# Optimization experiments

Measured on AMD Instinct MI355X. Metric: run time of the kernel, lower is better.

The kernel has to match this reference:

```python
import jax, jax.numpy as jnp
import numpy as np

NUM_HEAD = 8
NEG = -1e9

def _lin(x, W, b):
    return x @ W + b

def _attn(qx, kx, vx, mask, H):
    # qx:[B,S,D], kx/vx:[B,T,D], mask:[B,T] float (0/1). masked_fill BEFORE scale, per original.
    B, S, D = qx.shape
    T = kx.shape[1]
    dh = D // H
    qh = qx.reshape(B, S, H, dh).transpose(0, 2, 1, 3)
    kh = kx.reshape(B, T, H, dh).transpose(0, 2, 1, 3)
    vh = vx.reshape(B, T, H, dh).transpose(0, 2, 1, 3)
    s = jnp.einsum('bhsd,bhtd->bhst', qh, kh)
    s = jnp.where(mask[:, None, None, :] == 0, NEG, s) / jnp.sqrt(jnp.float32(dh))
    p = jax.nn.softmax(s, axis=-1)
    o = jnp.einsum('bhst,bhtd->bhsd', p, vh)
    return o.transpose(0, 2, 1, 3).reshape(B, S, D)

def _forward(v, q, c, v_mask, q_mask, c_mask,
             Wv4q, bv4q, Wq4v, bq4v, Wv, bv, Wq, bq, Wc, bc,
             m_v_k, m_v_v, m_c_k, m_c_v, Wvo, bvo, Wqo, bqo, Wco, bco):
    B = v.shape[0]
    D = Wvo.shape[0]
    H = NUM_HEAD
    # masked means -> gates
    v_mean = (v * v_mask[:, :, None]).sum(1) / v_mask.sum(1)[:, None]
    q_mean = (q * q_mask[:, :, None]).sum(1) / q_mask.sum(1)[:, None]
    v4q_gate = jax.nn.sigmoid(_lin(jax.nn.relu(v_mean), Wv4q, bv4q))[:, None, :]
    q4v_gate = jax.nn.sigmoid(_lin(jax.nn.relu(q_mean), Wq4v, bq4v))[:, None, :]
    # QKV projections (drop=0), masked
    v_trans = _lin(jax.nn.relu(v), Wv, bv) * v_mask[:, :, None]
    q_trans = _lin(jax.nn.relu(q), Wq, bq) * q_mask[:, :, None]
    c_trans = _lin(jax.nn.relu(c), Wc, bc) * c_mask[:, :, None]
    v_k, v_q, v_v = jnp.split(v_trans, 3, axis=2)
    q_k, q_q, q_v = jnp.split(q_trans, 3, axis=2)
    c_k, c_q, c_v = jnp.split(c_trans, 3, axis=2)
    # memory tokens: K scaled by sqrt(D), V scaled by sqrt(mv)=1 (faithful to original)
    sd = np.sqrt(D).astype(np.float32)
    m_vk = sd * jnp.broadcast_to(m_v_k, (B, 1, D))
    m_vv = 1.0 * jnp.broadcast_to(m_v_v, (B, 1, D))
    v_k = jnp.concatenate([m_vk, v_k], axis=1)
    v_v = jnp.concatenate([m_vv, v_v], axis=1)
    v_mask_m = jnp.concatenate([jnp.ones((B, 1), v_mask.dtype), v_mask], axis=1)
    m_ck = sd * jnp.broadcast_to(m_c_k, (B, 1, D))
    m_cv = 1.0 * jnp.broadcast_to(m_c_v, (B, 1, D))
    c_k = jnp.concatenate([m_ck, c_k], axis=1)
    c_v = jnp.concatenate([m_cv, c_v], axis=1)
    c_mask_m = jnp.concatenate([jnp.ones((B, 1), c_mask.dtype), c_mask], axis=1)
    # cross-modal gating of Q/K
    new_vq = (1 + q4v_gate) * v_q
    new_vk = (1 + q4v_gate) * v_k
    new_qq = (1 + v4q_gate) * q_q
    new_qk = (1 + v4q_gate) * q_k
    # multi-head attention (vectorized over heads; equivalent to the per-head loop)
    v_update = _attn(new_vq, new_vk, v_v, v_mask_m, H)
    q_update = _attn(new_qq, new_qk, q_v, q_mask, H)
    c_update = _attn(c_q, c_k, c_v, c_mask_m, H)
    updated_v = _lin(v + v_update, Wvo, bvo)
    updated_q = _lin(q + q_update, Wqo, bqo)
    updated_c = _lin(c + c_update, Wco, bco)
    return (updated_v, updated_q, updated_c)

def setup_inputs() -> dict:
    key = jax.random.key(0)
    ks = jax.random.split(key, 20)
    B, NO, ML, MLC, D = 32, 512, 256, 512, 1024
    s = 0.02
    def N(k, shape, sc=1.0):
        return jax.random.normal(k, shape, dtype=jnp.float32) * sc
    def M(k, b, S):
        m = (jax.random.uniform(k, (b, S)) < 0.85).astype(jnp.float32)
        return m.at[:, 0].set(1.0)  # guarantee nonzero mask sums
    return dict(
        v=N(ks[0], (B, NO, D)), q=N(ks[1], (B, ML, D)), c=N(ks[2], (B, MLC, D)),
        v_mask=M(ks[3], B, NO), q_mask=M(ks[4], B, ML), c_mask=M(ks[5], B, MLC),
        Wv4q=N(ks[6], (D, D), s), bv4q=jnp.zeros((D,), jnp.float32),
        Wq4v=N(ks[7], (D, D), s), bq4v=jnp.zeros((D,), jnp.float32),
        Wv=N(ks[8], (D, 3 * D), s), bv=jnp.zeros((3 * D,), jnp.float32),
        Wq=N(ks[9], (D, 3 * D), s), bq=jnp.zeros((3 * D,), jnp.float32),
        Wc=N(ks[10], (D, 3 * D), s), bc=jnp.zeros((3 * D,), jnp.float32),
        m_v_k=N(ks[11], (1, 1, D), s), m_v_v=N(ks[12], (1, 1, D), s),
        m_c_k=N(ks[13], (1, 1, D), s), m_c_v=N(ks[14], (1, 1, D), s),
        Wvo=N(ks[15], (D, D), s), bvo=jnp.zeros((D,), jnp.float32),
        Wqo=N(ks[16], (D, D), s), bqo=jnp.zeros((D,), jnp.float32),
        Wco=N(ks[17], (D, D), s), bco=jnp.zeros((D,), jnp.float32),
    )

def reference(v, q, c, v_mask, q_mask, c_mask,
              Wv4q, bv4q, Wq4v, bq4v, Wv, bv, Wq, bq, Wc, bc,
              m_v_k, m_v_v, m_c_k, m_c_v, Wvo, bvo, Wqo, bqo, Wco, bco):
    return _forward(v, q, c, v_mask, q_mask, c_mask,
                    Wv4q, bv4q, Wq4v, bq4v, Wv, bv, Wq, bq, Wc, bc,
                    m_v_k, m_v_v, m_c_k, m_c_v, Wvo, bvo, Wqo, bqo, Wco, bco)
```

## Files before the change

kernel.cpp:

```cpp
#include <hip/hip_runtime.h>
#include <hip/hip_bf16.h>

typedef __bf16 bf16;
typedef __bf16 bf16x8 __attribute__((ext_vector_type(8)));
typedef float  f32x4  __attribute__((ext_vector_type(4)));

__device__ __forceinline__ void gl2lds16(const bf16* g, bf16* l) {
    __builtin_amdgcn_global_load_lds((const __attribute__((address_space(1))) void*)g,
                                     (__attribute__((address_space(3))) void*)l,
                                     16, 0, 0);
}

__global__ void relu_cast_kernel(const float* __restrict__ x, bf16* __restrict__ y, int n8) {
    int i = blockIdx.x * 256 + threadIdx.x;
    if (i >= n8) return;
    const float4* xp = (const float4*)x + (size_t)i * 2;
    float4 a = xp[0], b = xp[1];
    bf16x8 o;
    o[0] = (bf16)fmaxf(a.x, 0.f); o[1] = (bf16)fmaxf(a.y, 0.f);
    o[2] = (bf16)fmaxf(a.z, 0.f); o[3] = (bf16)fmaxf(a.w, 0.f);
    o[4] = (bf16)fmaxf(b.x, 0.f); o[5] = (bf16)fmaxf(b.y, 0.f);
    o[6] = (bf16)fmaxf(b.z, 0.f); o[7] = (bf16)fmaxf(b.w, 0.f);
    *(bf16x8*)(y + (size_t)i * 8) = o;
}

__global__ void mean_kernel(const float* __restrict__ x, const float* __restrict__ mask,
                            float* __restrict__ mean, int S) {
    int b = blockIdx.y;
    int n = blockIdx.x * 256 + threadIdx.x;
    const float* xb = x + (size_t)b * S * 1024;
    const float* mb = mask + (size_t)b * S;
    float acc = 0.f, msum = 0.f;
    for (int s = 0; s < S; ++s) {
        float mk = mb[s];
        msum += mk;
        acc += mk * xb[(size_t)s * 1024 + n];
    }
    mean[b * 1024 + n] = acc / msum;
}

__global__ void gate_kernel(const float* __restrict__ mean, const float* __restrict__ W,
                            const float* __restrict__ bias, float* __restrict__ gate) {
    int b = blockIdx.y;
    int n = blockIdx.x * 256 + threadIdx.x;
    const float* mb = mean + b * 1024;
    float acc = 0.f;
    for (int k = 0; k < 1024; ++k) {
        float a = mb[k];
        a = a > 0.f ? a : 0.f;
        acc += a * W[(size_t)k * 1024 + n];
    }
    acc += bias[n];
    gate[b * 1024 + n] = 1.0f / (1.0f + __expf(-acc));
}

__global__ void transpose_kernel(const float* __restrict__ W, bf16* __restrict__ Wt,
                                 int K, int N) {
    __shared__ bf16 tile[32][33];
    int k0 = blockIdx.x * 32, n0 = blockIdx.y * 32;
    int tx = threadIdx.x, ty = threadIdx.y;
#pragma unroll
    for (int i = 0; i < 4; ++i)
        tile[ty * 4 + i][tx] = (bf16)W[(size_t)(k0 + ty * 4 + i) * N + n0 + tx];
    __syncthreads();
#pragma unroll
    for (int i = 0; i < 4; ++i)
        Wt[(size_t)(n0 + ty * 4 + i) * K + k0 + tx] = tile[tx][ty * 4 + i];
}

template <typename OutT>
__global__ void gemm_bt(const bf16* __restrict__ A, const bf16* __restrict__ Bt,
                        const float* __restrict__ bias, OutT* __restrict__ C,
                        int M, int N,
                        const float* __restrict__ mask,
                        const float* __restrict__ gate,
                        int s_shift)
{
    const int K = 1024;
    __shared__ __align__(16) bf16 Al[128 * 32];
    __shared__ __align__(16) bf16 Bl[128 * 32];

    int tid  = threadIdx.x;
    int lane = tid & 63, w = tid >> 6;
    int wm = w >> 1, wn = w & 1;
    int quad = lane >> 4, l16 = lane & 15;
    int bm = blockIdx.y, bn = blockIdx.x;

    const bf16* Ab = A  + (size_t)bm * 128 * K;
    const bf16* Bb = Bt + (size_t)bn * 128 * K;

    f32x4 acc[4][4];
    f32x4 zero = {0.f, 0.f, 0.f, 0.f};
#pragma unroll
    for (int i = 0; i < 4; ++i)
#pragma unroll
        for (int j = 0; j < 4; ++j) acc[i][j] = zero;

    for (int k0 = 0; k0 < K; k0 += 32) {
        __syncthreads();
#pragma unroll
        for (int p = 0; p < 2; ++p) {
            int c   = p * 256 + tid;
            int row = c >> 2, c8 = (c & 3) * 8;
            bf16* ldsb_a = Al + (size_t)(p * 256 + w * 64) * 8;
            bf16* ldsb_b = Bl + (size_t)(p * 256 + w * 64) * 8;
            gl2lds16(Ab + (size_t)row * K + k0 + c8, ldsb_a);
            gl2lds16(Bb + (size_t)row * K + k0 + c8, ldsb_b);
        }
        __syncthreads();

        bf16x8 af[4], bfr[4];
#pragma unroll
        for (int mt = 0; mt < 4; ++mt)
            af[mt] = *(const bf16x8*)&Al[(wm * 64 + mt * 16 + l16) * 32 + quad * 8];
#pragma unroll
        for (int nt = 0; nt < 4; ++nt)
            bfr[nt] = *(const bf16x8*)&Bl[(wn * 64 + nt * 16 + l16) * 32 + quad * 8];
#pragma unroll
        for (int mt = 0; mt < 4; ++mt)
#pragma unroll
            for (int nt = 0; nt < 4; ++nt)
                acc[mt][nt] = __builtin_amdgcn_mfma_f32_16x16x32_bf16(
                    af[mt], bfr[nt], acc[mt][nt], 0, 0, 0);
    }

#pragma unroll
    for (int mt = 0; mt < 4; ++mt) {
#pragma unroll
        for (int nt = 0; nt < 4; ++nt) {
#pragma unroll
            for (int r = 0; r < 4; ++r) {
                int mrow = bm * 128 + wm * 64 + mt * 16 + quad * 4 + r;
                int ncol = bn * 128 + wn * 64 + nt * 16 + l16;
                float v = acc[mt][nt][r] + bias[ncol];
                if (mask) {
                    v *= mask[mrow];
                    if (gate && ncol < 2048) {
                        int b = mrow >> s_shift;
                        v *= 1.0f + gate[b * 1024 + (ncol & 1023)];
                    }
                }
                C[(size_t)mrow * N + ncol] = (OutT)v;
            }
        }
    }
}

__global__ __launch_bounds__(256)
void attn_kernel(const bf16* __restrict__ trans, const float* __restrict__ X,
                 bf16* __restrict__ upd, const float* __restrict__ mask,
                 const float* __restrict__ gate,
                 const float* __restrict__ mvk, const float* __restrict__ mvv,
                 int S, int T0, int has_mem)
{
    const int T = T0 + has_mem;
    const size_t rs = 3072;
    __shared__ __align__(16) bf16 Kl[64 * 128];
    __shared__ __align__(16) bf16 Vt[128 * 72];
    __shared__ __align__(16) bf16 Pl[4 * 16 * 72];

    int tid  = threadIdx.x;
    int lane = tid & 63, w = tid >> 6;
    int quad = lane >> 4, l16 = lane & 15;
    int st = blockIdx.x, h = blockIdx.y, b = blockIdx.z;
    int s0 = st * 64;
    const bf16* Tb = trans + (size_t)b * S * rs;

    bf16x8 qf[4];
    {
        const bf16* qp = Tb + (size_t)(s0 + w * 16 + l16) * rs + 1024 + h * 128 + quad * 8;
#pragma unroll
        for (int kk = 0; kk < 4; ++kk)
            qf[kk] = *(const bf16x8*)(qp + kk * 32);
    }

    float m_st[4], l_st[4];
    f32x4 o_acc[8];
    f32x4 zero = {0.f, 0.f, 0.f, 0.f};
#pragma unroll
    for (int r = 0; r < 4; ++r) { m_st[r] = -3.0e38f; l_st[r] = 0.f; }
#pragma unroll
    for (int n = 0; n < 8; ++n) o_acc[n] = zero;

    const float inv_sqrt = 0.08838834764831845f;
    int nT = (T + 63) >> 6;
    for (int kt = 0; kt < nT; ++kt) {
        int t0 = kt * 64;
        __syncthreads();

#pragma unroll
        for (int p = 0; p < 4; ++p) {
            int c = p * 256 + tid;
            int row = c >> 4;
            int c16 = ((c & 15) ^ (row & 7)) * 8;
            int t = t0 + row;
            int sr = has_mem ? (t - 1) : t;
            sr = sr < 0 ? 0 : sr;
            sr = sr > T0 - 1 ? T0 - 1 : sr;
            gl2lds16(Tb + (size_t)sr * rs + h * 128 + c16,
                     Kl + (size_t)(p * 256 + w * 64) * 8);
        }
#pragma unroll
        for (int i = 0; i < 4; ++i) {
            int chunk = i * 256 + tid;
            int tl = chunk >> 4;
            int d8 = (chunk & 15) * 8;
            int t = t0 + tl;
            bf16 vbuf[8];
            if (has_mem && t == 0) {
                const float* mp = mvv + h * 128 + d8;
#pragma unroll
                for (int j = 0; j < 8; ++j) vbuf[j] = (bf16)mp[j];
            } else {
                int sr = has_mem ? (t - 1) : t;
                sr = sr < 0 ? 0 : sr;
                sr = sr > T0 - 1 ? T0 - 1 : sr;
                bf16x8 vv = *(const bf16x8*)(Tb + (size_t)sr * rs + 2048 + h * 128 + d8);
#pragma unroll
                for (int j = 0; j < 8; ++j) vbuf[j] = vv[j];
            }
            int tswz = (((tl >> 3) ^ ((d8 >> 3) & 7)) << 3) + (tl & 7);
#pragma unroll
            for (int j = 0; j < 8; ++j)
                Vt[(d8 + j) * 72 + tswz] = vbuf[j];
        }
        __syncthreads();

        if (has_mem && kt == 0 && tid < 128) {
            float g = gate ? (1.0f + gate[b * 1024 + h * 128 + tid]) : 1.0f;
            Kl[tid] = (bf16)(32.0f * mvk[h * 128 + tid] * g);
        }
        __syncthreads();

        f32x4 accs[4];
#pragma unroll
        for (int tt = 0; tt < 4; ++tt) accs[tt] = zero;
#pragma unroll
        for (int kc = 0; kc < 128; kc += 32) {
            bf16x8 aq = qf[kc >> 5];
#pragma unroll
            for (int tt = 0; tt < 4; ++tt) {
                bf16x8 bk = *(const bf16x8*)&Kl[(tt * 16 + l16) * 128 +
                                                ((((kc >> 3) + quad) ^ (l16 & 7)) << 3)];
                accs[tt] = __builtin_amdgcn_mfma_f32_16x16x32_bf16(aq, bk, accs[tt], 0, 0, 0);
            }
        }

        float sv[4][4];
#pragma unroll
        for (int tt = 0; tt < 4; ++tt) {
            int t = t0 + tt * 16 + l16;
            float mk;
            if (t >= T)        mk = 0.f;
            else if (has_mem)  mk = (t == 0) ? 1.f : mask[b * T0 + t - 1];
            else               mk = mask[b * T0 + t];
#pragma unroll
            for (int r = 0; r < 4; ++r) {
                float x = accs[tt][r];
                x = (mk != 0.f) ? x : -1e9f;
                sv[tt][r] = x * inv_sqrt;
            }
        }

#pragma unroll
        for (int r = 0; r < 4; ++r) {
            float mx = fmaxf(fmaxf(sv[0][r], sv[1][r]), fmaxf(sv[2][r], sv[3][r]));
#pragma unroll
            for (int off = 1; off < 16; off <<= 1)
                mx = fmaxf(mx, __shfl_xor(mx, off, 64));
            float m_new = fmaxf(m_st[r], mx);
            float alpha = __expf(m_st[r] - m_new);
            float rsum = 0.f;
#pragma unroll
            for (int tt = 0; tt < 4; ++tt) {
                float p = __expf(sv[tt][r] - m_new);
                sv[tt][r] = p;
                rsum += p;
            }
#pragma unroll
            for (int off = 1; off < 16; off <<= 1)
                rsum += __shfl_xor(rsum, off, 64);
            l_st[r] = l_st[r] * alpha + rsum;
            m_st[r] = m_new;
#pragma unroll
            for (int n = 0; n < 8; ++n) o_acc[n][r] *= alpha;
        }

#pragma unroll
        for (int tt = 0; tt < 4; ++tt)
#pragma unroll
            for (int r = 0; r < 4; ++r)
                Pl[w * 1152 + (quad * 4 + r) * 72 + tt * 16 + l16] = (bf16)sv[tt][r];
        __asm__ volatile("s_waitcnt lgkmcnt(0)" ::: "memory");

#pragma unroll
        for (int kc = 0; kc < 64; kc += 32) {
            bf16x8 ap = *(const bf16x8*)&Pl[w * 1152 + l16 * 72 + kc + quad * 8];
#pragma unroll
            for (int n = 0; n < 8; ++n) {
                int d = n * 16 + l16;
                int ct = ((kc >> 3) + quad) ^ ((d >> 3) & 7);
                bf16x8 bv = *(const bf16x8*)&Vt[d * 72 + (ct << 3)];
                o_acc[n] = __builtin_amdgcn_mfma_f32_16x16x32_bf16(ap, bv, o_acc[n], 0, 0, 0);
            }
        }
    }

#pragma unroll
    for (int n = 0; n < 8; ++n) {
#pragma unroll
        for (int r = 0; r < 4; ++r) {
            int s = s0 + w * 16 + quad * 4 + r;
            int d = n * 16 + l16;
            size_t off = (size_t)(b * S + s) * 1024 + h * 128 + d;
            float val = o_acc[n][r] / l_st[r];
            upd[off] = (bf16)(X[off] + val);
        }
    }
}

extern "C" void kernel_launch(void* const* d_in, const int* in_sizes, int n_in,
                              void* d_out, int out_size, void* d_ws, size_t ws_size,
                              hipStream_t stream) {
    (void)in_sizes; (void)n_in; (void)out_size; (void)ws_size;
    const float* v      = (const float*)d_in[0];
    const float* q      = (const float*)d_in[1];
    const float* c      = (const float*)d_in[2];
    const float* v_mask = (const float*)d_in[3];
    const float* q_mask = (const float*)d_in[4];
    const float* c_mask = (const float*)d_in[5];
    const float* Wv4q = (const float*)d_in[6];
    const float* bv4q = (const float*)d_in[7];
    const float* Wq4v = (const float*)d_in[8];
    const float* bq4v = (const float*)d_in[9];
    const float* Wv   = (const float*)d_in[10];
    const float* bv   = (const float*)d_in[11];
    const float* Wq   = (const float*)d_in[12];
    const float* bq   = (const float*)d_in[13];
    const float* Wc   = (const float*)d_in[14];
    const float* bc   = (const float*)d_in[15];
    const float* mvk  = (const float*)d_in[16];
    const float* mvv  = (const float*)d_in[17];
    const float* mck  = (const float*)d_in[18];
    const float* mcv  = (const float*)d_in[19];
    const float* Wvo  = (const float*)d_in[20];
    const float* bvo  = (const float*)d_in[21];
    const float* Wqo  = (const float*)d_in[22];
    const float* bqo  = (const float*)d_in[23];
    const float* Wco  = (const float*)d_in[24];
    const float* bco  = (const float*)d_in[25];
    float* out = (float*)d_out;

    char* ws = (char*)d_ws;
    size_t o = 0;
    bf16*  reluV  = (bf16*)(ws + o); o += (size_t)16384 * 1024 * 2;
    bf16*  reluQ  = (bf16*)(ws + o); o += (size_t)8192  * 1024 * 2;
    bf16*  reluC  = (bf16*)(ws + o); o += (size_t)16384 * 1024 * 2;
    bf16*  WtV    = (bf16*)(ws + o); o += (size_t)3072 * 1024 * 2;
    bf16*  WtQ    = (bf16*)(ws + o); o += (size_t)3072 * 1024 * 2;
    bf16*  WtC    = (bf16*)(ws + o); o += (size_t)3072 * 1024 * 2;
    bf16*  WtVO   = (bf16*)(ws + o); o += (size_t)1024 * 1024 * 2;
    bf16*  WtQO   = (bf16*)(ws + o); o += (size_t)1024 * 1024 * 2;
    bf16*  WtCO   = (bf16*)(ws + o); o += (size_t)1024 * 1024 * 2;
    bf16*  transV = (bf16*)(ws + o); o += (size_t)16384 * 3072 * 2;
    bf16*  transQ = (bf16*)(ws + o); o += (size_t)8192  * 3072 * 2;
    bf16*  transC = (bf16*)(ws + o); o += (size_t)16384 * 3072 * 2;
    float* meanV  = (float*)(ws + o); o += (size_t)32 * 1024 * 4;
    float* meanQ  = (float*)(ws + o); o += (size_t)32 * 1024 * 4;
    float* gV4Q   = (float*)(ws + o); o += (size_t)32 * 1024 * 4;
    float* gQ4V   = (float*)(ws + o); o += (size_t)32 * 1024 * 4;
    bf16* updV = reluV;
    bf16* updQ = reluQ;
    bf16* updC = reluC;

    relu_cast_kernel<<<8192, 256, 0, stream>>>(v, reluV, 2097152);
    relu_cast_kernel<<<4096, 256, 0, stream>>>(q, reluQ, 1048576);
    relu_cast_kernel<<<8192, 256, 0, stream>>>(c, reluC, 2097152);

    mean_kernel<<<dim3(4, 32), 256, 0, stream>>>(v, v_mask, meanV, 512);
    mean_kernel<<<dim3(4, 32), 256, 0, stream>>>(q, q_mask, meanQ, 256);

    gate_kernel<<<dim3(4, 32), 256, 0, stream>>>(meanV, Wv4q, bv4q, gV4Q);
    gate_kernel<<<dim3(4, 32), 256, 0, stream>>>(meanQ, Wq4v, bq4v, gQ4V);

    transpose_kernel<<<dim3(32, 96), dim3(32, 8), 0, stream>>>(Wv,  WtV,  1024, 3072);
    transpose_kernel<<<dim3(32, 96), dim3(32, 8), 0, stream>>>(Wq,  WtQ,  1024, 3072);
    transpose_kernel<<<dim3(32, 96), dim3(32, 8), 0, stream>>>(Wc,  WtC,  1024, 3072);
    transpose_kernel<<<dim3(32, 32), dim3(32, 8), 0, stream>>>(Wvo, WtVO, 1024, 1024);
    transpose_kernel<<<dim3(32, 32), dim3(32, 8), 0, stream>>>(Wqo, WtQO, 1024, 1024);
    transpose_kernel<<<dim3(32, 32), dim3(32, 8), 0, stream>>>(Wco, WtCO, 1024, 1024);

    gemm_bt<bf16><<<dim3(24, 128), 256, 0, stream>>>(reluV, WtV, bv, transV, 16384, 3072, v_mask, gQ4V, 9);
    gemm_bt<bf16><<<dim3(24, 64),  256, 0, stream>>>(reluQ, WtQ, bq, transQ, 8192,  3072, q_mask, gV4Q, 8);
    gemm_bt<bf16><<<dim3(24, 128), 256, 0, stream>>>(reluC, WtC, bc, transC, 16384, 3072, c_mask, nullptr, 9);

    attn_kernel<<<dim3(8, 8, 32), 256, 0, stream>>>(transV, v, updV, v_mask, gQ4V, mvk, mvv, 512, 512, 1);
    attn_kernel<<<dim3(4, 8, 32), 256, 0, stream>>>(transQ, q, updQ, q_mask, nullptr, nullptr, nullptr, 256, 256, 0);
    attn_kernel<<<dim3(8, 8, 32), 256, 0, stream>>>(transC, c, updC, c_mask, nullptr, mck, mcv, 512, 512, 1);

    gemm_bt<float><<<dim3(8, 128), 256, 0, stream>>>(updV, WtVO, bvo, out,            16384, 1024, nullptr, nullptr, 0);
    gemm_bt<float><<<dim3(8, 64),  256, 0, stream>>>(updQ, WtQO, bqo, out + 16777216, 8192,  1024, nullptr, nullptr, 0);
    gemm_bt<float><<<dim3(8, 128), 256, 0, stream>>>(updC, WtCO, bco, out + 25165824, 16384, 1024, nullptr, nullptr, 0);
}
```

Baseline: 1.657 ms.

## Replace 128x128 GEMM with double-buffered 256x256 tile GEMM using swizzled LDS

The 128x128 single-buffered GEMM is replaced by a 256x256-tile kernel with 512 threads and 8x4 MFMA fragments per wave. It uses double-buffered LDS staging over a K step of 64, split into two 32-wide halves, with vmcnt-based barriers so the next tile's loads overlap the current MFMAs. It also adds an XOR swizzle on LDS columns and raises wave priority around the MFMA blocks. The goal is more data reuse per byte loaded, hidden global-load latency and fewer bank conflicts, at the cost of higher register pressure and fewer blocks for the small Q GEMMs.

```diff
diff --git a/kernel.cpp b/kernel.cpp
--- a/kernel.cpp
+++ b/kernel.cpp
@@ -9,6 +9,17 @@
     __builtin_amdgcn_global_load_lds((const __attribute__((address_space(1))) void*)g,
                                      (__attribute__((address_space(3))) void*)l,
                                      16, 0, 0);
+}
+
+__device__ __forceinline__ void vm_bar4() {
+    asm volatile("s_waitcnt vmcnt(4)" ::: "memory");
+    __builtin_amdgcn_s_barrier();
+    asm volatile("" ::: "memory");
+}
+__device__ __forceinline__ void vm_bar0() {
+    asm volatile("s_waitcnt vmcnt(0)" ::: "memory");
+    __builtin_amdgcn_s_barrier();
+    asm volatile("" ::: "memory");
 }
 
 __global__ void relu_cast_kernel(const float* __restrict__ x, bf16* __restrict__ y, int n8) {
@@ -69,78 +80,113 @@
 }
 
 template <typename OutT>
-__global__ void gemm_bt(const bf16* __restrict__ A, const bf16* __restrict__ Bt,
-                        const float* __restrict__ bias, OutT* __restrict__ C,
-                        int M, int N,
-                        const float* __restrict__ mask,
-                        const float* __restrict__ gate,
-                        int s_shift)
+__global__ __launch_bounds__(512, 2)
+void gemm256(const bf16* __restrict__ A, const bf16* __restrict__ Bt,
+             const float* __restrict__ bias, OutT* __restrict__ C,
+             int N,
+             const float* __restrict__ mask,
+             const float* __restrict__ gate,
+             int s_shift)
 {
-    const int K = 1024;
-    __shared__ __align__(16) bf16 Al[128 * 32];
-    __shared__ __align__(16) bf16 Bl[128 * 32];
-
-    int tid  = threadIdx.x;
-    int lane = tid & 63, w = tid >> 6;
-    int wm = w >> 1, wn = w & 1;
-    int quad = lane >> 4, l16 = lane & 15;
-    int bm = blockIdx.y, bn = blockIdx.x;
-
-    const bf16* Ab = A  + (size_t)bm * 128 * K;
-    const bf16* Bb = Bt + (size_t)bn * 128 * K;
-
-    f32x4 acc[4][4];
+    constexpr int KD = 1024;
+    constexpr int NT = 16;
+    __shared__ __align__(16) bf16 Ls[2][2][2][8192];
+
+    const int tid  = threadIdx.x;
+    const int lane = tid & 63, w = tid >> 6;
+    const int wm = w >> 2, wn = w & 3;
+    const int quad = lane >> 4, l16 = lane & 15;
+    const int bn = blockIdx.x, bm = blockIdx.y;
+
+    const bf16* Ab = A  + (size_t)bm * 256 * KD;
+    const bf16* Bb = Bt + (size_t)bn * 256 * KD;
+
+    const int srow   = tid >> 2;
+    const int schunk = tid & 3;
+    const int scol   = ((schunk ^ ((srow >> 1) & 3)) << 3);
+    const bf16* gA0 = Ab + (size_t)srow * KD + scol;
+    const bf16* gB0 = Bb + (size_t)srow * KD + scol;
+    const int ldst = w * 512;
+
+    const int cswz = ((quad ^ ((l16 >> 1) & 3)) << 3);
+    const int aoff = (wm * 128 + l16) * 32 + cswz;
+    const int boff = (wn * 64  + l16) * 32 + cswz;
+
+    f32x4 acc[8][4];
     f32x4 zero = {0.f, 0.f, 0.f, 0.f};
 #pragma unroll
-    for (int i = 0; i < 4; ++i)
+    for (int i = 0; i < 8; ++i)
 #pragma unroll
         for (int j = 0; j < 4; ++j) acc[i][j] = zero;
 
-    for (int k0 = 0; k0 < K; k0 += 32) {
-        __syncthreads();
-#pragma unroll
-        for (int p = 0; p < 2; ++p) {
-            int c   = p * 256 + tid;
-            int row = c >> 2, c8 = (c & 3) * 8;
-            bf16* ldsb_a = Al + (size_t)(p * 256 + w * 64) * 8;
-            bf16* ldsb_b = Bl + (size_t)(p * 256 + w * 64) * 8;
-            gl2lds16(Ab + (size_t)row * K + k0 + c8, ldsb_a);
-            gl2lds16(Bb + (size_t)row * K + k0 + c8, ldsb_b);
-        }
-        __syncthreads();
-
-        bf16x8 af[4], bfr[4];
-#pragma unroll
-        for (int mt = 0; mt < 4; ++mt)
-            af[mt] = *(const bf16x8*)&Al[(wm * 64 + mt * 16 + l16) * 32 + quad * 8];
-#pragma unroll
-        for (int nt = 0; nt < 4; ++nt)
-            bfr[nt] = *(const bf16x8*)&Bl[(wn * 64 + nt * 16 + l16) * 32 + quad * 8];
-#pragma unroll
-        for (int mt = 0; mt < 4; ++mt)
-#pragma unroll
-            for (int nt = 0; nt < 4; ++nt)
-                acc[mt][nt] = __builtin_amdgcn_mfma_f32_16x16x32_bf16(
-                    af[mt], bfr[nt], acc[mt][nt], 0, 0, 0);
-    }
-
-#pragma unroll
-    for (int mt = 0; mt < 4; ++mt) {
-#pragma unroll
-        for (int nt = 0; nt < 4; ++nt) {
+    auto STAGE = [&](int buf, int kk, int t) {
+        const bf16* ga = gA0 + t * 64 + kk * 32;
+        const bf16* gb = gB0 + t * 64 + kk * 32;
+        bf16* la = &Ls[buf][0][kk][ldst];
+        bf16* lb = &Ls[buf][1][kk][ldst];
+        gl2lds16(ga,              la);
+        gl2lds16(ga + 128 * KD,   la + 4096);
+        gl2lds16(gb,              lb);
+        gl2lds16(gb + 128 * KD,   lb + 4096);
+    };
+
+    auto COMPUTE = [&](int buf, int kk) {
+        const bf16* Ak = &Ls[buf][0][kk][0];
+        const bf16* Bk = &Ls[buf][1][kk][0];
+        bf16x8 af[8], bv[4];
+#pragma unroll
+        for (int mf = 0; mf < 8; ++mf)
+            af[mf] = *(const bf16x8*)&Ak[aoff + mf * 512];
+#pragma unroll
+        for (int nf = 0; nf < 4; ++nf)
+            bv[nf] = *(const bf16x8*)&Bk[boff + nf * 512];
+        __builtin_amdgcn_s_setprio(1);
+#pragma unroll
+        for (int mf = 0; mf < 8; ++mf)
+#pragma unroll
+            for (int nf = 0; nf < 4; ++nf)
+                acc[mf][nf] = __builtin_amdgcn_mfma_f32_16x16x32_bf16(
+                    af[mf], bv[nf], acc[mf][nf], 0, 0, 0);
+        __builtin_amdgcn_s_setprio(0);
+    };
+
+    STAGE(0, 0, 0);
+    STAGE(0, 1, 0);
+    vm_bar4();
+
+    int buf = 0;
+    for (int t = 0; t < NT - 1; ++t) {
+        STAGE(buf ^ 1, 0, t + 1);
+        COMPUTE(buf, 0);
+        vm_bar4();
+        STAGE(buf ^ 1, 1, t + 1);
+        COMPUTE(buf, 1);
+        vm_bar4();
+        buf ^= 1;
+    }
+    COMPUTE(buf, 0);
+    vm_bar0();
+    COMPUTE(buf, 1);
+
+#pragma unroll
+    for (int mf = 0; mf < 8; ++mf) {
+        int mrow0 = bm * 256 + wm * 128 + mf * 16 + quad * 4;
+#pragma unroll
+        for (int nf = 0; nf < 4; ++nf) {
+            int ncol = bn * 256 + wn * 64 + nf * 16 + l16;
+            float bs = bias[ncol];
 #pragma unroll
             for (int r = 0; r < 4; ++r) {
-                int mrow = bm * 128 + wm * 64 + mt * 16 + quad * 4 + r;
-                int ncol = bn * 128 + wn * 64 + nt * 16 + l16;
-                float v = acc[mt][nt][r] + bias[ncol];
+                int mr = mrow0 + r;
+                float vv = acc[mf][nf][r] + bs;
                 if (mask) {
-                    v *= mask[mrow];
+                    vv *= mask[mr];
                     if (gate && ncol < 2048) {
-                        int b = mrow >> s_shift;
-                        v *= 1.0f + gate[b * 1024 + (ncol & 1023)];
+                        int bb = mr >> s_shift;
+                        vv *= 1.0f + gate[bb * 1024 + (ncol & 1023)];
                     }
                 }
-                C[(size_t)mrow * N + ncol] = (OutT)v;
+                C[(size_t)mr * N + ncol] = (OutT)vv;
             }
         }
     }
@@ -300,8 +346,8 @@
             for (int n = 0; n < 8; ++n) {
                 int d = n * 16 + l16;
                 int ct = ((kc >> 3) + quad) ^ ((d >> 3) & 7);
-                bf16x8 bv = *(const bf16x8*)&Vt[d * 72 + (ct << 3)];
-                o_acc[n] = __builtin_amdgcn_mfma_f32_16x16x32_bf16(ap, bv, o_acc[n], 0, 0, 0);
+                bf16x8 bvv = *(const bf16x8*)&Vt[d * 72 + (ct << 3)];
+                o_acc[n] = __builtin_amdgcn_mfma_f32_16x16x32_bf16(ap, bvv, o_acc[n], 0, 0, 0);
             }
         }
     }
@@ -390,15 +436,15 @@
     transpose_kernel<<<dim3(32, 32), dim3(32, 8), 0, stream>>>(Wqo, WtQO, 1024, 1024);
     transpose_kernel<<<dim3(32, 32), dim3(32, 8), 0, stream>>>(Wco, WtCO, 1024, 1024);
 
-    gemm_bt<bf16><<<dim3(24, 128), 256, 0, stream>>>(reluV, WtV, bv, transV, 16384, 3072, v_mask, gQ4V, 9);
-    gemm_bt<bf16><<<dim3(24, 64),  256, 0, stream>>>(reluQ, WtQ, bq, transQ, 8192,  3072, q_mask, gV4Q, 8);
-    gemm_bt<bf16><<<dim3(24, 128), 256, 0, stream>>>(reluC, WtC, bc, transC, 16384, 3072, c_mask, nullptr, 9);
+    gemm256<bf16><<<dim3(12, 64), 512, 0, stream>>>(reluV, WtV, bv, transV, 3072, v_mask, gQ4V, 9);
+    gemm256<bf16><<<dim3(12, 32), 512, 0, stream>>>(reluQ, WtQ, bq, transQ, 3072, q_mask, gV4Q, 8);
+    gemm256<bf16><<<dim3(12, 64), 512, 0, stream>>>(reluC, WtC, bc, transC, 3072, c_mask, nullptr, 9);
 
     attn_kernel<<<dim3(8, 8, 32), 256, 0, stream>>>(transV, v, updV, v_mask, gQ4V, mvk, mvv, 512, 512, 1);
     attn_kernel<<<dim3(4, 8, 32), 256, 0, stream>>>(transQ, q, updQ, q_mask, nullptr, nullptr, nullptr, 256, 256, 0);
     attn_kernel<<<dim3(8, 8, 32), 256, 0, stream>>>(transC, c, updC, c_mask, nullptr, mck, mcv, 512, 512, 1);
 
-    gemm_bt<float><<<dim3(8, 128), 256, 0, stream>>>(updV, WtVO, bvo, out,            16384, 1024, nullptr, nullptr, 0);
-    gemm_bt<float><<<dim3(8, 64),  256, 0, stream>>>(updQ, WtQO, bqo, out + 16777216, 8192,  1024, nullptr, nullptr, 0);
-    gemm_bt<float><<<dim3(8, 128), 256, 0, stream>>>(updC, WtCO, bco, out + 25165824, 16384, 1024, nullptr, nullptr, 0);
-}
+    gemm256<float><<<dim3(4, 64), 512, 0, stream>>>(updV, WtVO, bvo, out,            1024, nullptr, nullptr, 0);
+    gemm256<float><<<dim3(4, 32), 512, 0, stream>>>(updQ, WtQO, bqo, out + 16777216, 1024, nullptr, nullptr, 0);
+    gemm256<float><<<dim3(4, 64), 512, 0, stream>>>(updC, WtCO, bco, out + 25165824, 1024, nullptr, nullptr, 0);
+}
```

After: 1.635 ms. No clear change (-1.3%).
